# Kernel tuning notes

Hardware: AMD Instinct MI355X
Metric: run time of the kernel (lower is better)

Reference implementation:

```python
import jax, jax.numpy as jnp
import numpy as np

DIM = 256
NUM_HEADS = 8
HEAD_DIM = DIM // NUM_HEADS


def setup_inputs() -> dict:
    key = jax.random.key(0)
    k1, k2, k3, k4 = jax.random.split(key, 4)
    B, C, H, W = 16, DIM, 64, 64
    x = jax.random.normal(k1, (B, C, H, W), dtype=jnp.float32)
    # 1x1 convs as dense weight matrices [out_ch, in_ch]
    Wqkv = jax.random.normal(k2, (3 * DIM, DIM), dtype=jnp.float32) * (DIM ** -0.5)
    Wproj = jax.random.normal(k3, (DIM, DIM), dtype=jnp.float32) * (DIM ** -0.5)
    bproj = jax.random.normal(k4, (DIM,), dtype=jnp.float32) * 0.01
    return {"x": x, "Wqkv": Wqkv, "Wproj": Wproj, "bproj": bproj}


def reference(x, Wqkv, Wproj, bproj):
    B, C, H, W = x.shape
    N = H * W
    hd = C // NUM_HEADS

    # qkv: 1x1 conv (no bias) == channel matmul
    qkv = jnp.einsum('oc,bchw->bohw', Wqkv, x)  # [B, 3C, H, W]
    q, k, v = jnp.split(qkv, 3, axis=1)

    def to_heads(t):
        # b (h d) x y -> b h (x y) d
        return t.reshape(B, NUM_HEADS, hd, N).transpose(0, 1, 3, 2)

    q, k, v = to_heads(q), to_heads(k), to_heads(v)  # [B, h, N, d]

    # linear attention feature map + per-token normalization over d
    q = jax.nn.elu(q) + 1.0
    k = jax.nn.elu(k) + 1.0
    q = q / jnp.sum(q, axis=-1, keepdims=True)
    k = k / jnp.sum(k, axis=-1, keepdims=True)

    kv = jnp.einsum('bhnd,bhne->bhde', k, v)   # [B, h, d, d]
    out = jnp.einsum('bhnd,bhde->bhne', q, kv)  # [B, h, N, d]

    # b h (x y) d -> b (h d) x y
    out = out.transpose(0, 1, 3, 2).reshape(B, C, H, W)

    # proj: 1x1 conv with bias; drop_path is identity in eval mode
    out = jnp.einsum('oc,bchw->bohw', Wproj, out) + bproj[None, :, None, None]
    return out + x
```

## Files before the change

kernel.cpp:

```cpp
#include <hip/hip_runtime.h>
#include <stdint.h>
#include <stddef.h>

#define DIM   256
#define NH    8
#define HD    32
#define BATCH 16
#define NTOK  4096

typedef __attribute__((ext_vector_type(8))) short short8;
typedef __attribute__((ext_vector_type(4))) float f32x4;

__device__ __forceinline__ unsigned short f2bf(float x){
  unsigned u = __float_as_uint(x);
  u += 0x7fffu + ((u >> 16) & 1u);
  return (unsigned short)(u >> 16);
}
__device__ __forceinline__ float elu1(float v){
  return (v > 0.f) ? (v + 1.f) : __expf(v);
}
__device__ __forceinline__ void gload_lds16(const void* g, void* lds){
  __builtin_amdgcn_global_load_lds(
      (const __attribute__((address_space(1))) unsigned int*)g,
      (__attribute__((address_space(3))) unsigned int*)lds, 16, 0, 0);
}

__global__ __launch_bounds__(256) void k_prep(const float* __restrict__ x,
                                              unsigned short* __restrict__ xt,
                                              const float* __restrict__ wqkv,
                                              unsigned short* __restrict__ wq_bf){
  const int t = threadIdx.x;
  if (blockIdx.z < 16){
    __shared__ float tile[64][65];
    const int b = blockIdx.z, c0 = blockIdx.y * 64, n0 = blockIdx.x * 64;
    const float* xb = x + (size_t)b * DIM * NTOK;
    #pragma unroll
    for (int p = 0; p < 4; p++){
      int idx = t + p * 256;
      int row = idx >> 4;
      int col = (idx & 15) << 2;
      float4 v = *(const float4*)(xb + (size_t)(c0 + row) * NTOK + n0 + col);
      tile[row][col] = v.x; tile[row][col+1] = v.y; tile[row][col+2] = v.z; tile[row][col+3] = v.w;
    }
    __syncthreads();
    unsigned short* xtb = xt + (size_t)b * NTOK * DIM;
    #pragma unroll
    for (int p = 0; p < 4; p++){
      int idx = t + p * 256;
      int nl = idx >> 4;
      int cl = (idx & 15) << 2;
      ushort4 o;
      o.x = f2bf(tile[cl+0][nl]); o.y = f2bf(tile[cl+1][nl]);
      o.z = f2bf(tile[cl+2][nl]); o.w = f2bf(tile[cl+3][nl]);
      *(ushort4*)(xtb + (size_t)(n0 + nl) * DIM + c0 + cl) = o;
    }
  } else {
    const int blk = blockIdx.y * 64 + blockIdx.x;
    if (blk >= 192) return;
    int i = blk * 256 + t;
    int row = i >> 6;
    int c4 = (i & 63) * 4;
    int dst;
    if (row < 256)      dst = row;
    else if (row < 512){ int p = (row - 256) >> 6; int s = (row - 256) & 63; dst = 256 + p*128 + s; }
    else               { int p = (row - 512) >> 6; int s = (row - 512) & 63; dst = 256 + p*128 + 64 + s; }
    float4 v = *(const float4*)(wqkv + (size_t)row * DIM + c4);
    ushort4 o = { f2bf(v.x), f2bf(v.y), f2bf(v.z), f2bf(v.w) };
    *(ushort4*)(wq_bf + (size_t)dst * DIM + c4) = o;
  }
}

__global__ __launch_bounds__(512, 1) void k_qkv11(const unsigned short* __restrict__ wbf,
                                                  const unsigned short* __restrict__ xt,
                                                  unsigned short* __restrict__ qn,
                                                  float* __restrict__ kvp){
  __shared__ __align__(16) unsigned short sh[33792];
  unsigned short* bsh = sh + 16384;
  const int t = threadIdx.x;
  const int w = t >> 6, l = t & 63;
  const int t16 = l & 15, quad = l >> 4;
  const int wm = w >> 1, wn = w & 1;
  const int bid = blockIdx.x;
  const int super = bid / 48;
  const int rem = bid - super * 48;
  const int m = rem >> 3, lx = rem & 7;
  const int chunk = super * 8 + lx;
  const int b = chunk >> 4, nt2 = chunk & 15;
  const int o0 = m * 128;
  const bool isQ = (o0 < 256);
  const unsigned short* Bb = xt + ((size_t)b * NTOK + (size_t)nt2 * 256) * DIM;
  const int rowL = (w*16 + t16) * DIM + quad*8;

  short8 a_reg[4][2][2];
  {
    const unsigned short* srcA = wbf + (size_t)(o0 + w*16 + t16) * DIM + quad*8;
    #pragma unroll
    for (int c = 0; c < 4; c++){
      gload_lds16(srcA + c*64,      sh + (w*8 + c*2 + 0)*512);
      gload_lds16(srcA + c*64 + 32, sh + (w*8 + c*2 + 1)*512);
    }
    asm volatile("s_waitcnt vmcnt(0)" ::: "memory");
    __builtin_amdgcn_s_barrier();
    #pragma unroll
    for (int c = 0; c < 4; c++)
      #pragma unroll
      for (int i = 0; i < 2; i++)
        #pragma unroll
        for (int kk = 0; kk < 2; kk++)
          a_reg[c][i][kk] = *(const short8*)(sh + ((wm*2 + i)*8 + c*2 + kk)*512 + l*8);
    asm volatile("s_waitcnt lgkmcnt(0)" ::: "memory");
    __builtin_amdgcn_s_barrier();
  }

#define STAGE(ss) { \
    const unsigned short* srcB = Bb + (size_t)(((ss) >> 2)*128) * DIM + rowL + ((ss) & 3)*64; \
    unsigned short* db = sh + ((ss) & 1) * 8192; \
    gload_lds16(srcB,      db + (w*2 + 0)*512); \
    gload_lds16(srcB + 32, db + (w*2 + 1)*512); }

  STAGE(0); STAGE(1);

  f32x4 acc[2][4];
  #pragma unroll
  for (int i = 0; i < 2; i++)
    #pragma unroll
    for (int j = 0; j < 4; j++){ acc[i][j][0]=0.f; acc[i][j][1]=0.f; acc[i][j][2]=0.f; acc[i][j][3]=0.f; }
  f32x4 kvacc;
  kvacc[0]=0.f; kvacc[1]=0.f; kvacc[2]=0.f; kvacc[3]=0.f;

  #pragma unroll
  for (int s = 0; s < 8; s++){
    if (s < 4)       { asm volatile("s_waitcnt vmcnt(2)" ::: "memory"); }
    else if (s < 6)  { if (isQ) { asm volatile("s_waitcnt vmcnt(6)" ::: "memory"); }
                       else     { asm volatile("s_waitcnt vmcnt(2)" ::: "memory"); } }
    else if (s == 6) { asm volatile("s_waitcnt vmcnt(2)" ::: "memory"); }
    else             { asm volatile("s_waitcnt vmcnt(0)" ::: "memory"); }
    __builtin_amdgcn_s_barrier();
    const unsigned short* bufc = sh + (s & 1) * 8192;
    __builtin_amdgcn_s_setprio(1);
    #pragma unroll
    for (int kk = 0; kk < 2; kk++){
      short8 bb[4];
      #pragma unroll
      for (int j = 0; j < 4; j++) bb[j] = *(const short8*)(bufc + ((wn*4 + j)*2 + kk)*512 + l*8);
      #pragma unroll
      for (int i = 0; i < 2; i++)
        #pragma unroll
        for (int j = 0; j < 4; j++)
          acc[i][j] = __builtin_amdgcn_mfma_f32_16x16x32_bf16(a_reg[s&3][i][kk], bb[j], acc[i][j], 0, 0, 0);
    }
    __builtin_amdgcn_s_setprio(0);
    __builtin_amdgcn_s_barrier();
    if (s < 6) STAGE(s + 2);

    if ((s & 3) == 3){
      const int n0 = (nt2*2 + (s >> 2)) * 128;
      if (isQ || wm < 2){
        #pragma unroll
        for (int i = 0; i < 2; i++)
          #pragma unroll
          for (int j = 0; j < 4; j++)
            #pragma unroll
            for (int r = 0; r < 4; r++) acc[i][j][r] = elu1(acc[i][j][r]);
        float sc[4];
        #pragma unroll
        for (int j = 0; j < 4; j++){
          float v = 0.f;
          #pragma unroll
          for (int i = 0; i < 2; i++)
            #pragma unroll
            for (int r = 0; r < 4; r++) v += acc[i][j][r];
          v += __shfl_xor(v, 16);
          v += __shfl_xor(v, 32);
          sc[j] = 1.0f / v;
        }
        #pragma unroll
        for (int i = 0; i < 2; i++)
          #pragma unroll
          for (int j = 0; j < 4; j++){
            float inv = sc[j];
            #pragma unroll
            for (int r = 0; r < 4; r++) acc[i][j][r] *= inv;
          }
      }
      if (isQ){
        #pragma unroll
        for (int i = 0; i < 2; i++)
          #pragma unroll
          for (int j = 0; j < 4; j++){
            int n_l = wn*64 + j*16 + t16;
            int o_l0 = wm*32 + i*16 + quad*4;
            ushort4 pk = { f2bf(acc[i][j][0]), f2bf(acc[i][j][1]),
                           f2bf(acc[i][j][2]), f2bf(acc[i][j][3]) };
            *(ushort4*)(bsh + n_l*136 + o_l0) = pk;
          }
        asm volatile("s_waitcnt lgkmcnt(0)" ::: "memory");
        __builtin_amdgcn_s_barrier();
        unsigned short* dst = qn + (size_t)b * NTOK * DIM;
        #pragma unroll
        for (int p2 = 0; p2 < 4; p2++){
          int gg = t + p2 * 512;
          int n_l = gg >> 4, c = gg & 15;
          uint4 v = *(const uint4*)(bsh + n_l*136 + c*8);
          *(uint4*)(dst + (size_t)(n0 + n_l) * DIM + o0 + c*8) = v;
        }
      } else {
        #pragma unroll
        for (int i = 0; i < 2; i++)
          #pragma unroll
          for (int j = 0; j < 4; j++){
            int n_l = wn*64 + j*16 + t16;
            #pragma unroll
            for (int r = 0; r < 4; r++){
              int o_l = wm*32 + i*16 + quad*4 + r;
              bsh[o_l*136 + n_l] = f2bf(acc[i][j][r]);
            }
          }
        asm volatile("s_waitcnt lgkmcnt(0)" ::: "memory");
        __builtin_amdgcn_s_barrier();
        const int hl = w >> 2, dh = (w >> 1) & 1, eh = w & 1;
        const unsigned short* kbase = bsh + (hl*32 + dh*16) * 136;
        const unsigned short* vbase = bsh + (64 + hl*32 + eh*16) * 136;
        #pragma unroll
        for (int kk2 = 0; kk2 < 4; kk2++){
          int nn = kk2*32 + quad*8;
          short8 afrag = *(const short8*)(kbase + t16*136 + nn);
          short8 bfrag = *(const short8*)(vbase + t16*136 + nn);
          kvacc = __builtin_amdgcn_mfma_f32_16x16x32_bf16(afrag, bfrag, kvacc, 0, 0, 0);
        }
      }
      if (s == 3){
        #pragma unroll
        for (int i = 0; i < 2; i++)
          #pragma unroll
          for (int j = 0; j < 4; j++){ acc[i][j][0]=0.f; acc[i][j][1]=0.f; acc[i][j][2]=0.f; acc[i][j][3]=0.f; }
      }
    }
  }
#undef STAGE

  if (!isQ){
    const int pp = (o0 >> 7) - 2;
    const int hl = w >> 2, dh = (w >> 1) & 1, eh = w & 1;
    float* dst = kvp + ((size_t)((b*8 + pp*2 + hl) * 16 + nt2)) * 1024;
    #pragma unroll
    for (int r = 0; r < 4; r++)
      dst[(dh*16 + quad*4 + r)*32 + eh*16 + t16] = kvacc[r];
  }
}

__global__ __launch_bounds__(256) void k_M(const float* __restrict__ kvp,
                                           const float* __restrict__ wproj,
                                           unsigned short* __restrict__ M){
  __shared__ float kvL[1024];
  __shared__ float wpL[8192];
  const int t = threadIdx.x;
  const int h = blockIdx.x, b = blockIdx.y;
  const float* pbase = kvp + (size_t)((b*8 + h) * 16) * 1024;
  {
    float4 a = {0.f,0.f,0.f,0.f};
    #pragma unroll
    for (int p = 0; p < 16; p++){
      float4 v = *(const float4*)(pbase + (size_t)p*1024 + t*4);
      a.x += v.x; a.y += v.y; a.z += v.z; a.w += v.w;
    }
    *(float4*)(kvL + t*4) = a;
  }
  #pragma unroll
  for (int p = 0; p < 8; p++){
    int idx = t + p * 256;
    int o = idx >> 3, e4 = idx & 7;
    *(float4*)(wpL + o*32 + e4*4) = *(const float4*)(wproj + (size_t)o * DIM + h*32 + e4*4);
  }
  __syncthreads();
  float wr[32];
  #pragma unroll
  for (int e = 0; e < 32; e++) wr[e] = wpL[t*32 + e];
  unsigned short md[32];
  #pragma unroll
  for (int d = 0; d < 32; d++){
    float a = 0.f;
    #pragma unroll
    for (int e = 0; e < 32; e++) a += wr[e] * kvL[d*32 + e];
    md[d] = f2bf(a);
  }
  unsigned short* dst = M + (size_t)b * 65536 + (size_t)t * DIM + h*32;
  #pragma unroll
  for (int q = 0; q < 4; q++) *(uint4*)(dst + q*8) = *(const uint4*)(md + q*8);
}

__global__ __launch_bounds__(512, 2) void k_out6(const unsigned short* __restrict__ M,
                                                 const unsigned short* __restrict__ qn,
                                                 const float* __restrict__ x,
                                                 const float* __restrict__ bproj,
                                                 float* __restrict__ out){
  __shared__ __align__(16) unsigned short As[16384];
  __shared__ __align__(16) unsigned short Bs[8192];
  const int t = threadIdx.x;
  const int w = t >> 6, l = t & 63;
  const int t16 = l & 15, quad = l >> 4;
  const int wm = w >> 1, wn = w & 1;
  const int bid = blockIdx.x;
  const int super = bid >> 4;
  const int rem = bid & 15;
  const int m = rem >> 3, lx = rem & 7;
  const int g = super * 8 + lx;
  const int nt = g >> 4, b = g & 15;
  const int o0 = m * 128, n0 = nt * 256;
  const unsigned short* A = qn + (size_t)b * NTOK * DIM;
  const unsigned short* Bm = M + (size_t)b * 65536;

  f32x4 acc[4][4];
  #pragma unroll
  for (int i = 0; i < 4; i++)
    #pragma unroll
    for (int j = 0; j < 4; j++){ acc[i][j][0]=0.f; acc[i][j][1]=0.f; acc[i][j][2]=0.f; acc[i][j][3]=0.f; }

  for (int k0 = 0; k0 < 256; k0 += 64){
    __syncthreads();
    #pragma unroll
    for (int s4 = 0; s4 < 4; s4++){
      int sl = w*4 + s4;
      int tile = sl >> 1, kk = sl & 1;
      gload_lds16(A + (size_t)(n0 + tile*16 + t16) * DIM + k0 + kk*32 + quad*8, As + sl*512);
    }
    #pragma unroll
    for (int s2 = 0; s2 < 2; s2++){
      int sl = w*2 + s2;
      int tile = sl >> 1, kk = sl & 1;
      gload_lds16(Bm + (size_t)(o0 + tile*16 + t16) * DIM + k0 + kk*32 + quad*8, Bs + sl*512);
    }
    __syncthreads();
    #pragma unroll
    for (int kk = 0; kk < 2; kk++){
      short8 a[4], bb[4];
      #pragma unroll
      for (int i = 0; i < 4; i++) a[i]  = *(const short8*)(As + ((wm*4 + i)*2 + kk) * 512 + l * 8);
      #pragma unroll
      for (int j = 0; j < 4; j++) bb[j] = *(const short8*)(Bs + ((wn*4 + j)*2 + kk) * 512 + l * 8);
      #pragma unroll
      for (int i = 0; i < 4; i++)
        #pragma unroll
        for (int j = 0; j < 4; j++)
          acc[i][j] = __builtin_amdgcn_mfma_f32_16x16x32_bf16(a[i], bb[j], acc[i][j], 0, 0, 0);
    }
  }

  const float* xb = x + (size_t)b * DIM * NTOK;
  float* ob = out + (size_t)b * DIM * NTOK;
  #pragma unroll
  for (int j = 0; j < 4; j++){
    int o = o0 + wn*64 + j*16 + t16;
    float bias = bproj[o];
    #pragma unroll
    for (int i = 0; i < 4; i++){
      int n = n0 + wm*64 + i*16 + quad*4;
      float4 xv = *(const float4*)(xb + (size_t)o * NTOK + n);
      float4 res = { acc[i][j][0] + bias + xv.x,
                     acc[i][j][1] + bias + xv.y,
                     acc[i][j][2] + bias + xv.z,
                     acc[i][j][3] + bias + xv.w };
      *(float4*)(ob + (size_t)o * NTOK + n) = res;
    }
  }
}

extern "C" void kernel_launch(void* const* d_in, const int* in_sizes, int n_in,
                              void* d_out, int out_size, void* d_ws, size_t ws_size,
                              hipStream_t stream){
  const float* x     = (const float*)d_in[0];
  const float* wqkv  = (const float*)d_in[1];
  const float* wproj = (const float*)d_in[2];
  const float* bproj = (const float*)d_in[3];
  float* out = (float*)d_out;
  char* ws = (char*)d_ws;

  unsigned short* xt   = (unsigned short*)(ws);
  unsigned short* qn   = (unsigned short*)(ws + ((size_t)32 << 20));
  float* kvp           = (float*)(ws + ((size_t)64 << 20));
  unsigned short* M    = (unsigned short*)(ws + ((size_t)80 << 20));
  unsigned short* wqbf = (unsigned short*)(ws + ((size_t)82 << 20));

  k_prep  <<<dim3(64, 4, 17), 256, 0, stream>>>(x, xt, wqkv, wqbf);
  k_qkv11 <<<dim3(1536), 512, 0, stream>>>(wqbf, xt, qn, kvp);
  k_M     <<<dim3(8, 16), 256, 0, stream>>>(kvp, wproj, M);
  k_out6  <<<dim3(512), 512, 0, stream>>>(M, qn, x, bproj, out);
}
```

Baseline: 219.9 us.

## Enlarge QKV GEMM tile to 256x256 and stream both operands through LDS

The QKV projection kernel now computes a 256-output by 256-token tile per block (768 blocks instead of 1536). It stops keeping the weight slice in registers and double-buffers both weight and activation K-slices through LDS. Each wave holds 8x4 MFMA accumulators, and the K/V blocks run a larger per-tile kv reduction over 256 tokens. The aim is more arithmetic per byte of LDS and global traffic and fewer blocks. The cost is much higher register pressure, twice the LDS, and fewer blocks to fill the CUs.

Result: no change. 219.9 us (-0.0%).

```diff
diff --git a/kernel.cpp b/kernel.cpp
--- a/kernel.cpp
+++ b/kernel.cpp
@@ -70,182 +70,175 @@
   }
 }
 
-__global__ __launch_bounds__(512, 1) void k_qkv11(const unsigned short* __restrict__ wbf,
+__device__ __forceinline__ void stage_step(const unsigned short* __restrict__ A,
+                                           const unsigned short* __restrict__ B,
+                                           unsigned short* buf, int k0,
+                                           int w, int t16, int quad){
+  #pragma unroll
+  for (int c = 0; c < 4; c++){
+    int s = w*4 + c;
+    int f = s >> 1, kk = s & 1;
+    size_t off = (size_t)(f*16 + t16) * DIM + k0 + kk*32 + quad*8;
+    gload_lds16(A + off, buf + s*512);
+    gload_lds16(B + off, buf + 16384 + s*512);
+  }
+}
+
+__global__ __launch_bounds__(512, 1) void k_qkv12(const unsigned short* __restrict__ wbf,
                                                   const unsigned short* __restrict__ xt,
                                                   unsigned short* __restrict__ qn,
                                                   float* __restrict__ kvp){
-  __shared__ __align__(16) unsigned short sh[33792];
-  unsigned short* bsh = sh + 16384;
+  __shared__ __align__(16) unsigned short sh[67584];
   const int t = threadIdx.x;
   const int w = t >> 6, l = t & 63;
   const int t16 = l & 15, quad = l >> 4;
-  const int wm = w >> 1, wn = w & 1;
+  const int wm = w >> 2, wn = w & 3;
   const int bid = blockIdx.x;
-  const int super = bid / 48;
-  const int rem = bid - super * 48;
+  const int super = bid / 24;
+  const int rem = bid - super * 24;
   const int m = rem >> 3, lx = rem & 7;
   const int chunk = super * 8 + lx;
-  const int b = chunk >> 4, nt2 = chunk & 15;
-  const int o0 = m * 128;
-  const bool isQ = (o0 < 256);
-  const unsigned short* Bb = xt + ((size_t)b * NTOK + (size_t)nt2 * 256) * DIM;
-  const int rowL = (w*16 + t16) * DIM + quad*8;
-
-  short8 a_reg[4][2][2];
-  {
-    const unsigned short* srcA = wbf + (size_t)(o0 + w*16 + t16) * DIM + quad*8;
-    #pragma unroll
-    for (int c = 0; c < 4; c++){
-      gload_lds16(srcA + c*64,      sh + (w*8 + c*2 + 0)*512);
-      gload_lds16(srcA + c*64 + 32, sh + (w*8 + c*2 + 1)*512);
-    }
-    asm volatile("s_waitcnt vmcnt(0)" ::: "memory");
+  const int b = chunk >> 4, nt = chunk & 15;
+  const int o0 = m * 256, n0 = nt * 256;
+  const bool isQ = (m == 0);
+  const unsigned short* A = wbf + (size_t)o0 * DIM;
+  const unsigned short* B = xt + ((size_t)b * NTOK + n0) * DIM;
+
+  stage_step(A, B, sh,         0, w, t16, quad);
+  stage_step(A, B, sh + 32768, 64, w, t16, quad);
+
+  f32x4 acc[8][4];
+  #pragma unroll
+  for (int i = 0; i < 8; i++)
+    #pragma unroll
+    for (int j = 0; j < 4; j++){ acc[i][j][0]=0.f; acc[i][j][1]=0.f; acc[i][j][2]=0.f; acc[i][j][3]=0.f; }
+
+  #pragma unroll
+  for (int s = 0; s < 4; s++){
+    if (s < 3) { asm volatile("s_waitcnt vmcnt(8)" ::: "memory"); }
+    else       { asm volatile("s_waitcnt vmcnt(0)" ::: "memory"); }
     __builtin_amdgcn_s_barrier();
-    #pragma unroll
-    for (int c = 0; c < 4; c++)
-      #pragma unroll
-      for (int i = 0; i < 2; i++)
-        #pragma unroll
-        for (int kk = 0; kk < 2; kk++)
-          a_reg[c][i][kk] = *(const short8*)(sh + ((wm*2 + i)*8 + c*2 + kk)*512 + l*8);
+    const unsigned short* buf = sh + (s & 1) * 32768;
+    #pragma unroll
+    for (int kk = 0; kk < 2; kk++){
+      short8 av[8], bv[4];
+      #pragma unroll
+      for (int i = 0; i < 8; i++) av[i] = *(const short8*)(buf + ((wm*8 + i)*2 + kk)*512 + l*8);
+      #pragma unroll
+      for (int j = 0; j < 4; j++) bv[j] = *(const short8*)(buf + 16384 + ((wn*4 + j)*2 + kk)*512 + l*8);
+      #pragma unroll
+      for (int i = 0; i < 8; i++)
+        #pragma unroll
+        for (int j = 0; j < 4; j++)
+          acc[i][j] = __builtin_amdgcn_mfma_f32_16x16x32_bf16(av[i], bv[j], acc[i][j], 0, 0, 0);
+    }
+    __builtin_amdgcn_s_barrier();
+    if (s < 2) stage_step(A, B, sh + (s & 1)*32768, (s + 2)*64, w, t16, quad);
+  }
+  unsigned short* bsh = sh;
+
+  if (isQ){
+    #pragma unroll
+    for (int i = 0; i < 8; i++)
+      #pragma unroll
+      for (int j = 0; j < 4; j++)
+        #pragma unroll
+        for (int r = 0; r < 4; r++) acc[i][j][r] = elu1(acc[i][j][r]);
+    #pragma unroll
+    for (int hh = 0; hh < 4; hh++)
+      #pragma unroll
+      for (int j = 0; j < 4; j++){
+        float v = 0.f;
+        #pragma unroll
+        for (int ii = 0; ii < 2; ii++)
+          #pragma unroll
+          for (int r = 0; r < 4; r++) v += acc[hh*2 + ii][j][r];
+        v += __shfl_xor(v, 16);
+        v += __shfl_xor(v, 32);
+        float inv = 1.0f / v;
+        #pragma unroll
+        for (int ii = 0; ii < 2; ii++)
+          #pragma unroll
+          for (int r = 0; r < 4; r++) acc[hh*2 + ii][j][r] *= inv;
+      }
+    #pragma unroll
+    for (int i = 0; i < 8; i++)
+      #pragma unroll
+      for (int j = 0; j < 4; j++){
+        int n_l = wn*64 + j*16 + t16;
+        int o_l0 = wm*128 + i*16 + quad*4;
+        ushort4 pk = { f2bf(acc[i][j][0]), f2bf(acc[i][j][1]),
+                       f2bf(acc[i][j][2]), f2bf(acc[i][j][3]) };
+        *(ushort4*)(bsh + n_l*264 + o_l0) = pk;
+      }
     asm volatile("s_waitcnt lgkmcnt(0)" ::: "memory");
     __builtin_amdgcn_s_barrier();
-  }
-
-#define STAGE(ss) { \
-    const unsigned short* srcB = Bb + (size_t)(((ss) >> 2)*128) * DIM + rowL + ((ss) & 3)*64; \
-    unsigned short* db = sh + ((ss) & 1) * 8192; \
-    gload_lds16(srcB,      db + (w*2 + 0)*512); \
-    gload_lds16(srcB + 32, db + (w*2 + 1)*512); }
-
-  STAGE(0); STAGE(1);
-
-  f32x4 acc[2][4];
-  #pragma unroll
-  for (int i = 0; i < 2; i++)
-    #pragma unroll
-    for (int j = 0; j < 4; j++){ acc[i][j][0]=0.f; acc[i][j][1]=0.f; acc[i][j][2]=0.f; acc[i][j][3]=0.f; }
-  f32x4 kvacc;
-  kvacc[0]=0.f; kvacc[1]=0.f; kvacc[2]=0.f; kvacc[3]=0.f;
-
-  #pragma unroll
-  for (int s = 0; s < 8; s++){
-    if (s < 4)       { asm volatile("s_waitcnt vmcnt(2)" ::: "memory"); }
-    else if (s < 6)  { if (isQ) { asm volatile("s_waitcnt vmcnt(6)" ::: "memory"); }
-                       else     { asm volatile("s_waitcnt vmcnt(2)" ::: "memory"); } }
-    else if (s == 6) { asm volatile("s_waitcnt vmcnt(2)" ::: "memory"); }
-    else             { asm volatile("s_waitcnt vmcnt(0)" ::: "memory"); }
+    unsigned short* dst = qn + (size_t)b * NTOK * DIM;
+    #pragma unroll
+    for (int p2 = 0; p2 < 16; p2++){
+      int idx = t + p2 * 512;
+      int n_l = idx >> 5, c16 = idx & 31;
+      uint4 v = *(const uint4*)(bsh + n_l*264 + c16*8);
+      *(uint4*)(dst + (size_t)(n0 + n_l) * DIM + c16*8) = v;
+    }
+  } else {
+    #pragma unroll
+    for (int i = 0; i < 4; i++)
+      #pragma unroll
+      for (int j = 0; j < 4; j++)
+        #pragma unroll
+        for (int r = 0; r < 4; r++) acc[i][j][r] = elu1(acc[i][j][r]);
+    #pragma unroll
+    for (int hh = 0; hh < 2; hh++)
+      #pragma unroll
+      for (int j = 0; j < 4; j++){
+        float v = 0.f;
+        #pragma unroll
+        for (int ii = 0; ii < 2; ii++)
+          #pragma unroll
+          for (int r = 0; r < 4; r++) v += acc[hh*2 + ii][j][r];
+        v += __shfl_xor(v, 16);
+        v += __shfl_xor(v, 32);
+        float inv = 1.0f / v;
+        #pragma unroll
+        for (int ii = 0; ii < 2; ii++)
+          #pragma unroll
+          for (int r = 0; r < 4; r++) acc[hh*2 + ii][j][r] *= inv;
+      }
+    #pragma unroll
+    for (int i = 0; i < 8; i++)
+      #pragma unroll
+      for (int j = 0; j < 4; j++){
+        int n_l = wn*64 + j*16 + t16;
+        #pragma unroll
+        for (int r = 0; r < 4; r++){
+          int o_l = wm*128 + i*16 + quad*4 + r;
+          bsh[o_l*264 + n_l] = f2bf(acc[i][j][r]);
+        }
+      }
+    asm volatile("s_waitcnt lgkmcnt(0)" ::: "memory");
     __builtin_amdgcn_s_barrier();
-    const unsigned short* bufc = sh + (s & 1) * 8192;
-    __builtin_amdgcn_s_setprio(1);
-    #pragma unroll
-    for (int kk = 0; kk < 2; kk++){
-      short8 bb[4];
-      #pragma unroll
-      for (int j = 0; j < 4; j++) bb[j] = *(const short8*)(bufc + ((wn*4 + j)*2 + kk)*512 + l*8);
-      #pragma unroll
-      for (int i = 0; i < 2; i++)
-        #pragma unroll
-        for (int j = 0; j < 4; j++)
-          acc[i][j] = __builtin_amdgcn_mfma_f32_16x16x32_bf16(a_reg[s&3][i][kk], bb[j], acc[i][j], 0, 0, 0);
-    }
-    __builtin_amdgcn_s_setprio(0);
-    __builtin_amdgcn_s_barrier();
-    if (s < 6) STAGE(s + 2);
-
-    if ((s & 3) == 3){
-      const int n0 = (nt2*2 + (s >> 2)) * 128;
-      if (isQ || wm < 2){
-        #pragma unroll
-        for (int i = 0; i < 2; i++)
-          #pragma unroll
-          for (int j = 0; j < 4; j++)
-            #pragma unroll
-            for (int r = 0; r < 4; r++) acc[i][j][r] = elu1(acc[i][j][r]);
-        float sc[4];
-        #pragma unroll
-        for (int j = 0; j < 4; j++){
-          float v = 0.f;
-          #pragma unroll
-          for (int i = 0; i < 2; i++)
-            #pragma unroll
-            for (int r = 0; r < 4; r++) v += acc[i][j][r];
-          v += __shfl_xor(v, 16);
-          v += __shfl_xor(v, 32);
-          sc[j] = 1.0f / v;
-        }
-        #pragma unroll
-        for (int i = 0; i < 2; i++)
-          #pragma unroll
-          for (int j = 0; j < 4; j++){
-            float inv = sc[j];
-            #pragma unroll
-            for (int r = 0; r < 4; r++) acc[i][j][r] *= inv;
-          }
-      }
-      if (isQ){
-        #pragma unroll
-        for (int i = 0; i < 2; i++)
-          #pragma unroll
-          for (int j = 0; j < 4; j++){
-            int n_l = wn*64 + j*16 + t16;
-            int o_l0 = wm*32 + i*16 + quad*4;
-            ushort4 pk = { f2bf(acc[i][j][0]), f2bf(acc[i][j][1]),
-                           f2bf(acc[i][j][2]), f2bf(acc[i][j][3]) };
-            *(ushort4*)(bsh + n_l*136 + o_l0) = pk;
-          }
-        asm volatile("s_waitcnt lgkmcnt(0)" ::: "memory");
-        __builtin_amdgcn_s_barrier();
-        unsigned short* dst = qn + (size_t)b * NTOK * DIM;
-        #pragma unroll
-        for (int p2 = 0; p2 < 4; p2++){
-          int gg = t + p2 * 512;
-          int n_l = gg >> 4, c = gg & 15;
-          uint4 v = *(const uint4*)(bsh + n_l*136 + c*8);
-          *(uint4*)(dst + (size_t)(n0 + n_l) * DIM + o0 + c*8) = v;
-        }
-      } else {
-        #pragma unroll
-        for (int i = 0; i < 2; i++)
-          #pragma unroll
-          for (int j = 0; j < 4; j++){
-            int n_l = wn*64 + j*16 + t16;
-            #pragma unroll
-            for (int r = 0; r < 4; r++){
-              int o_l = wm*32 + i*16 + quad*4 + r;
-              bsh[o_l*136 + n_l] = f2bf(acc[i][j][r]);
-            }
-          }
-        asm volatile("s_waitcnt lgkmcnt(0)" ::: "memory");
-        __builtin_amdgcn_s_barrier();
-        const int hl = w >> 2, dh = (w >> 1) & 1, eh = w & 1;
-        const unsigned short* kbase = bsh + (hl*32 + dh*16) * 136;
-        const unsigned short* vbase = bsh + (64 + hl*32 + eh*16) * 136;
-        #pragma unroll
-        for (int kk2 = 0; kk2 < 4; kk2++){
-          int nn = kk2*32 + quad*8;
-          short8 afrag = *(const short8*)(kbase + t16*136 + nn);
-          short8 bfrag = *(const short8*)(vbase + t16*136 + nn);
-          kvacc = __builtin_amdgcn_mfma_f32_16x16x32_bf16(afrag, bfrag, kvacc, 0, 0, 0);
-        }
-      }
-      if (s == 3){
-        #pragma unroll
-        for (int i = 0; i < 2; i++)
-          #pragma unroll
-          for (int j = 0; j < 4; j++){ acc[i][j][0]=0.f; acc[i][j][1]=0.f; acc[i][j][2]=0.f; acc[i][j][3]=0.f; }
-      }
-    }
-  }
-#undef STAGE
-
-  if (!isQ){
-    const int pp = (o0 >> 7) - 2;
-    const int hl = w >> 2, dh = (w >> 1) & 1, eh = w & 1;
-    float* dst = kvp + ((size_t)((b*8 + pp*2 + hl) * 16 + nt2)) * 1024;
-    #pragma unroll
-    for (int r = 0; r < 4; r++)
-      dst[(dh*16 + quad*4 + r)*32 + eh*16 + t16] = kvacc[r];
+    #pragma unroll
+    for (int task = 0; task < 2; task++){
+      const int tt = w + task*8;
+      const int q = tt >> 3, hl = (tt >> 2) & 1, dh = (tt >> 1) & 1, eh = tt & 1;
+      f32x4 kvacc;
+      kvacc[0]=0.f; kvacc[1]=0.f; kvacc[2]=0.f; kvacc[3]=0.f;
+      const unsigned short* kbase = bsh + (q*128 + hl*32 + dh*16 + t16) * 264;
+      const unsigned short* vbase = bsh + (q*128 + 64 + hl*32 + eh*16 + t16) * 264;
+      #pragma unroll
+      for (int kk2 = 0; kk2 < 8; kk2++){
+        int nn = kk2*32 + quad*8;
+        short8 afrag = *(const short8*)(kbase + nn);
+        short8 bfrag = *(const short8*)(vbase + nn);
+        kvacc = __builtin_amdgcn_mfma_f32_16x16x32_bf16(afrag, bfrag, kvacc, 0, 0, 0);
+      }
+      const int pp_g = (m - 1)*2 + q;
+      float* dst = kvp + ((size_t)((b*8 + pp_g*2 + hl) * 16 + nt)) * 1024;
+      #pragma unroll
+      for (int r = 0; r < 4; r++)
+        dst[(dh*16 + quad*4 + r)*32 + eh*16 + t16] = kvacc[r];
+    }
   }
 }
 
@@ -382,7 +375,7 @@
   unsigned short* wqbf = (unsigned short*)(ws + ((size_t)82 << 20));
 
   k_prep  <<<dim3(64, 4, 17), 256, 0, stream>>>(x, xt, wqkv, wqbf);
-  k_qkv11 <<<dim3(1536), 512, 0, stream>>>(wqbf, xt, qn, kvp);
+  k_qkv12 <<<dim3(768), 512, 0, stream>>>(wqbf, xt, qn, kvp);
   k_M     <<<dim3(8, 16), 256, 0, stream>>>(kvp, wproj, M);
   k_out6  <<<dim3(512), 512, 0, stream>>>(M, qn, x, bproj, out);
 }
```
